# Kernel optimization log

Hardware: AMD Instinct MI355X
Metric: run time of the kernel (lower is better)

Reference implementation:

```python
import jax, jax.numpy as jnp
import numpy as np

B, H, S, D = 8, 16, 1024, 128

def setup_inputs() -> dict:
    key = jax.random.key(0)
    kq, kk, kv = jax.random.split(key, 3)
    q = jax.random.normal(kq, (B, H, S, D), dtype=jnp.float32)
    k = jax.random.normal(kk, (B, H, S, D), dtype=jnp.float32)
    v = jax.random.normal(kv, (B, H, S, D), dtype=jnp.float32)
    return {"q": q, "k": k, "v": v}

def reference(q, k, v):
    dims = q.shape[-1]
    # scores[..., j, i] = sum_k q[..., j, k] * k_[..., i, k]; note scale is 1/dims (not 1/sqrt(dims))
    scores = jnp.einsum('bhjd,bhid->bhji', q, k) / dims
    probs = jax.nn.softmax(scores, axis=-1)
    out = jnp.einsum('bhji,bhid->bhjd', probs, v)
    return out
```

## Files before the change

kernel.cpp:

```cpp
#include <hip/hip_runtime.h>

#define S_LEN 1024
#define D_DIM 128
#define KVBLK 32
#define BH_N 128

typedef __attribute__((ext_vector_type(8))) short short8;
typedef __attribute__((ext_vector_type(4))) short short4v;
typedef __attribute__((ext_vector_type(4))) float f32x4;
typedef __attribute__((ext_vector_type(16))) float f32x16;
typedef __attribute__((ext_vector_type(4))) unsigned int uint4v;

__device__ __forceinline__ unsigned short f2bf(float f) {
  union { float f; unsigned u; } x; x.f = f;
  unsigned r = x.u + 0x7fffu + ((x.u >> 16) & 1u);
  return (unsigned short)(r >> 16);
}

__device__ __forceinline__ short8 pack8(float4 a, float4 b) {
  short8 f;
  f[0] = (short)f2bf(a.x); f[1] = (short)f2bf(a.y);
  f[2] = (short)f2bf(a.z); f[3] = (short)f2bf(a.w);
  f[4] = (short)f2bf(b.x); f[5] = (short)f2bf(b.y);
  f[6] = (short)f2bf(b.z); f[7] = (short)f2bf(b.w);
  return f;
}

__device__ __forceinline__ void gload_lds16(const void* g, void* l) {
  __builtin_amdgcn_global_load_lds(
      (const __attribute__((address_space(1))) unsigned int*)g,
      (__attribute__((address_space(3))) unsigned int*)l, 16, 0, 0);
}

__device__ __forceinline__ short8 packP(const f32x16 sacc, const int c, float& l_r) {
  float p0 = exp2f(fminf(sacc[8 * c + 0], 80.f));
  float p1 = exp2f(fminf(sacc[8 * c + 1], 80.f));
  unsigned w0;
  asm("v_cvt_pk_bf16_f32 %0, %1, %2" : "=v"(w0) : "v"(p0), "v"(p1));
  float p2 = exp2f(fminf(sacc[8 * c + 2], 80.f));
  float p3 = exp2f(fminf(sacc[8 * c + 3], 80.f));
  unsigned w1;
  asm("v_cvt_pk_bf16_f32 %0, %1, %2" : "=v"(w1) : "v"(p2), "v"(p3));
  l_r += (p0 + p1) + (p2 + p3);
  float p4 = exp2f(fminf(sacc[8 * c + 4], 80.f));
  float p5 = exp2f(fminf(sacc[8 * c + 5], 80.f));
  unsigned w2;
  asm("v_cvt_pk_bf16_f32 %0, %1, %2" : "=v"(w2) : "v"(p4), "v"(p5));
  float p6 = exp2f(fminf(sacc[8 * c + 6], 80.f));
  float p7 = exp2f(fminf(sacc[8 * c + 7], 80.f));
  unsigned w3;
  asm("v_cvt_pk_bf16_f32 %0, %1, %2" : "=v"(w3) : "v"(p6), "v"(p7));
  l_r += (p4 + p5) + (p6 + p7);
  asm volatile("v_permlane32_swap_b32 %0, %1" : "+v"(w0), "+v"(w2));
  asm volatile("v_permlane32_swap_b32 %0, %1" : "+v"(w1), "+v"(w3));
  uint4v pw;
  pw[0] = w0; pw[1] = w1; pw[2] = w2; pw[3] = w3;
  return __builtin_bit_cast(short8, pw);
}

__global__ __launch_bounds__(256) void conv_k(const float* __restrict__ in,
                                              unsigned short* __restrict__ out,
                                              int n8) {
  int i = blockIdx.x * 256 + threadIdx.x;
  int stride = gridDim.x * 256;
  for (; i < n8; i += stride) {
    float4 a = ((const float4*)in)[i * 2];
    float4 b = ((const float4*)in)[i * 2 + 1];
    ((short8*)out)[i] = pack8(a, b);
  }
}

__global__ __launch_bounds__(256) void conv_vt(const float* __restrict__ v,
                                               unsigned short* __restrict__ vt) {
  __shared__ unsigned short tile[64][72];
  int b = blockIdx.x;
  int d0 = (b & 1) * 64;
  int s0 = ((b >> 1) & 15) * 64;
  int bh = b >> 5;
  int t = threadIdx.x;
  #pragma unroll
  for (int i = 0; i < 4; ++i) {
    int s = (t >> 4) + i * 16;
    int dl = (t & 15) * 4;
    float4 x = *(const float4*)(v + ((size_t)(bh * S_LEN) + s0 + s) * D_DIM + d0 + dl);
    tile[s][dl + 0] = f2bf(x.x); tile[s][dl + 1] = f2bf(x.y);
    tile[s][dl + 2] = f2bf(x.z); tile[s][dl + 3] = f2bf(x.w);
  }
  __syncthreads();
  #pragma unroll
  for (int i = 0; i < 2; ++i) {
    int j = i * 256 + t;
    int dl = j >> 3, sc = j & 7;
    short8 w;
    #pragma unroll
    for (int q = 0; q < 8; ++q) w[q] = (short)tile[sc * 8 + q][dl];
    *(short8*)(vt + ((size_t)(bh * D_DIM) + d0 + dl) * S_LEN + s0 + sc * 8) = w;
  }
}

__global__ __launch_bounds__(256, 2) void attn_main(
    const float* __restrict__ qg, const unsigned short* __restrict__ kbf,
    const unsigned short* __restrict__ vtbf, float* __restrict__ og) {
  __shared__ unsigned short K_lds[2][KVBLK * D_DIM];
  __shared__ unsigned short VT_lds[2][D_DIM * KVBLK];

  const int tid = threadIdx.x;
  const int lane = tid & 63;
  const int wid = tid >> 6;
  const int l31 = lane & 31;
  const int hi = lane >> 5;

  const int bid = blockIdx.x;
  const int bh = (bid & 7) | ((bid >> 5) << 3);
  const int qt = (bid >> 3) & 3;

  const size_t base = (size_t)bh * (S_LEN * D_DIM);
  const int qw = qt * 256 + wid * 64;

  short8 qfA[8], qfB[8];
  {
    const float s = 0.0078125f * 1.44269504088896f;
    const float* qpA = qg + base + (size_t)(qw + l31) * D_DIM + hi * 8;
    const float* qpB = qpA + 32 * D_DIM;
    #pragma unroll
    for (int c = 0; c < 8; ++c) {
      float4 a = *(const float4*)(qpA + c * 16);
      float4 b = *(const float4*)(qpA + c * 16 + 4);
      a.x *= s; a.y *= s; a.z *= s; a.w *= s;
      b.x *= s; b.y *= s; b.z *= s; b.w *= s;
      qfA[c] = pack8(a, b);
      float4 e = *(const float4*)(qpB + c * 16);
      float4 f = *(const float4*)(qpB + c * 16 + 4);
      e.x *= s; e.y *= s; e.z *= s; e.w *= s;
      f.x *= s; f.y *= s; f.z *= s; f.w *= s;
      qfB[c] = pack8(e, f);
    }
  }

  float lA = 0.f, lB = 0.f;
  f32x16 oA[4], oB[4];
  #pragma unroll
  for (int dt = 0; dt < 4; ++dt)
    #pragma unroll
    for (int r = 0; r < 16; ++r) { oA[dt][r] = 0.f; oB[dt][r] = 0.f; }

  const char* kbB = (const char*)(kbf + base);
  const char* vtB = (const char*)(vtbf + (size_t)bh * (D_DIM * S_LEN));

  int koffA, koffB, voff;
  {
    int r0 = wid * 8 + (lane >> 4);
    int c = lane & 15;
    koffA = (r0 * D_DIM + ((c ^ (r0 & 7)) * 8)) * 2;
    int r1 = r0 + 4;
    koffB = (r1 * D_DIM + ((c ^ (r1 & 7)) * 8)) * 2;
    int d0 = wid * 32 + (lane >> 2);
    int c2 = lane & 3;
    voff = (d0 * S_LEN + ((c2 ^ (lane >> 4)) * 8)) * 2;
  }
  const int KRB = l31 * 256 + ((hi ^ (l31 & 7)) << 4);
  const int VRB = l31 * 64 + ((hi ^ ((l31 >> 2) & 3)) << 4);

  #define STAGE(buf, tnext)                                                    \
    {                                                                          \
      const char* ks = kbB + (tnext) * (KVBLK * D_DIM * 2);                    \
      gload_lds16(ks + koffA, &K_lds[buf][(wid * 8) * D_DIM]);                 \
      gload_lds16(ks + koffB, &K_lds[buf][(wid * 8 + 4) * D_DIM]);             \
      const char* vs = vtB + (tnext) * (KVBLK * 2);                            \
      gload_lds16(vs + voff, &VT_lds[buf][(wid * 32) * KVBLK]);                \
      gload_lds16(vs + voff + 16 * S_LEN * 2,                                  \
                  &VT_lds[buf][(wid * 32 + 16) * KVBLK]);                      \
    }

  STAGE(0, 0);
  __syncthreads();

  for (int t = 0; t < S_LEN / KVBLK; ++t) {
    const int cur = t & 1;
    if (t + 1 < S_LEN / KVBLK) STAGE(cur ^ 1, t + 1);

    const char* kl = (const char*)&K_lds[cur][0];
    const char* vl = (const char*)&VT_lds[cur][0];

    f32x16 sA, sB;
    #pragma unroll
    for (int r = 0; r < 16; ++r) { sA[r] = 0.f; sB[r] = 0.f; }

    __builtin_amdgcn_s_setprio(1);
    #pragma unroll
    for (int c = 0; c < 8; ++c) {
      short8 kf = *(const short8*)(kl + (KRB ^ (c << 5)));
      sA = __builtin_amdgcn_mfma_f32_32x32x16_bf16(kf, qfA[c], sA, 0, 0, 0);
      sB = __builtin_amdgcn_mfma_f32_32x32x16_bf16(kf, qfB[c], sB, 0, 0, 0);
    }
    __builtin_amdgcn_s_setprio(0);

    short8 paA0 = packP(sA, 0, lA);
    short8 paA1 = packP(sA, 1, lA);
    short8 paB0 = packP(sB, 0, lB);
    short8 paB1 = packP(sB, 1, lB);

    __builtin_amdgcn_s_setprio(1);
    {
      const int vx0 = VRB;
      #pragma unroll
      for (int dt = 0; dt < 4; ++dt) {
        short8 vf = *(const short8*)(vl + vx0 + dt * 2048);
        oA[dt] = __builtin_amdgcn_mfma_f32_32x32x16_bf16(paA0, vf, oA[dt], 0, 0, 0);
        oB[dt] = __builtin_amdgcn_mfma_f32_32x32x16_bf16(paB0, vf, oB[dt], 0, 0, 0);
      }
      const int vx1 = VRB ^ 32;
      #pragma unroll
      for (int dt = 0; dt < 4; ++dt) {
        short8 vf = *(const short8*)(vl + vx1 + dt * 2048);
        oA[dt] = __builtin_amdgcn_mfma_f32_32x32x16_bf16(paA1, vf, oA[dt], 0, 0, 0);
        oB[dt] = __builtin_amdgcn_mfma_f32_32x32x16_bf16(paB1, vf, oB[dt], 0, 0, 0);
      }
    }
    __builtin_amdgcn_s_setprio(0);
    __syncthreads();
  }

  float lsA = lA + __shfl_xor(lA, 32);
  float liA = 1.0f / lsA;
  float lsB = lB + __shfl_xor(lB, 32);
  float liB = 1.0f / lsB;
  #pragma unroll
  for (int r = 0; r < 16; ++r) {
    int qr = (r & 3) + 8 * (r >> 2) + 4 * hi;
    float lvA = __shfl(liA, qr, 64);
    float lvB = __shfl(liB, qr, 64);
    #pragma unroll
    for (int dt = 0; dt < 4; ++dt) {
      og[base + (size_t)(qw + qr) * D_DIM + dt * 32 + l31] = oA[dt][r] * lvA;
      og[base + (size_t)(qw + 32 + qr) * D_DIM + dt * 32 + l31] = oB[dt][r] * lvB;
    }
  }
}

__global__ __launch_bounds__(256) void attn_fused(
    const float* __restrict__ qg, const float* __restrict__ kg,
    const float* __restrict__ vg, float* __restrict__ og) {
  __shared__ unsigned short K_lds[64 * D_DIM];
  __shared__ unsigned short VT_lds[D_DIM * 64];
  __shared__ unsigned short P_lds[4][16 * 64];

  const int tid = threadIdx.x;
  const int lane = tid & 63;
  const int wid = tid >> 6;
  const int l15 = lane & 15;
  const int lg = lane >> 4;

  const int bid = blockIdx.x;
  const int bh = (bid & 7) | ((bid >> 7) << 3);
  const int qt = (bid >> 3) & 15;

  const size_t base = (size_t)bh * (S_LEN * D_DIM);
  const int qw = qt * 64 + wid * 16;

  short8 qf[4];
  {
    const float* qp = qg + base + (size_t)(qw + l15) * D_DIM + lg * 8;
    #pragma unroll
    for (int c = 0; c < 4; ++c) {
      float4 a = *(const float4*)(qp + c * 32);
      float4 b = *(const float4*)(qp + c * 32 + 4);
      const float s = 0.0078125f;
      a.x *= s; a.y *= s; a.z *= s; a.w *= s;
      b.x *= s; b.y *= s; b.z *= s; b.w *= s;
      qf[c] = pack8(a, b);
    }
  }

  float m_r[4], l_r[4];
  f32x4 o_acc[8];
  #pragma unroll
  for (int r = 0; r < 4; ++r) { m_r[r] = -INFINITY; l_r[r] = 0.f; }
  #pragma unroll
  for (int dt = 0; dt < 8; ++dt) o_acc[dt] = (f32x4){0.f, 0.f, 0.f, 0.f};

  for (int kv0 = 0; kv0 < S_LEN; kv0 += 64) {
    {
      const float* kb = kg + base + (size_t)kv0 * D_DIM;
      #pragma unroll
      for (int c = tid; c < 64 * D_DIM / 8; c += 256) {
        int row = c >> 4, dc = c & 15;
        const float* p = kb + row * D_DIM + dc * 8;
        float4 a = *(const float4*)p;
        float4 b = *(const float4*)(p + 4);
        int sidx = row * 128 + ((dc * 8) ^ ((row & 7) << 3));
        *(short8*)&K_lds[sidx] = pack8(a, b);
      }
    }
    {
      const float* vb = vg + base + (size_t)kv0 * D_DIM;
      #pragma unroll
      for (int u = tid; u < (64 / 4) * (D_DIM / 4); u += 256) {
        int ib = u & 15;
        int db = u >> 4;
        const float* p = vb + (ib * 4) * D_DIM + db * 4;
        float rr[4][4];
        #pragma unroll
        for (int c = 0; c < 4; ++c) {
          float4 t = *(const float4*)(p + c * D_DIM);
          rr[c][0] = t.x; rr[c][1] = t.y; rr[c][2] = t.z; rr[c][3] = t.w;
        }
        #pragma unroll
        for (int j = 0; j < 4; ++j) {
          short4v w;
          w[0] = (short)f2bf(rr[0][j]); w[1] = (short)f2bf(rr[1][j]);
          w[2] = (short)f2bf(rr[2][j]); w[3] = (short)f2bf(rr[3][j]);
          int row = db * 4 + j;
          int sidx = row * 64 + ((ib * 4) ^ ((row & 7) << 3));
          *(short4v*)&VT_lds[sidx] = w;
        }
      }
    }
    __syncthreads();

    f32x4 sacc[4];
    #pragma unroll
    for (int tc = 0; tc < 4; ++tc) sacc[tc] = (f32x4){0.f, 0.f, 0.f, 0.f};
    #pragma unroll
    for (int tc = 0; tc < 4; ++tc) {
      int row = tc * 16 + l15;
      #pragma unroll
      for (int ck = 0; ck < 4; ++ck) {
        int sidx = row * 128 + ((ck * 32 + lg * 8) ^ ((row & 7) << 3));
        short8 kf = *(const short8*)&K_lds[sidx];
        sacc[tc] = __builtin_amdgcn_mfma_f32_16x16x32_bf16(qf[ck], kf, sacc[tc], 0, 0, 0);
      }
    }

    float alpha[4], ps[4];
    #pragma unroll
    for (int r = 0; r < 4; ++r) {
      float a = fmaxf(fmaxf(sacc[0][r], sacc[1][r]), fmaxf(sacc[2][r], sacc[3][r]));
      a = fmaxf(a, __shfl_xor(a, 1));
      a = fmaxf(a, __shfl_xor(a, 2));
      a = fmaxf(a, __shfl_xor(a, 4));
      a = fmaxf(a, __shfl_xor(a, 8));
      float mn = fmaxf(m_r[r], a);
      alpha[r] = __expf(m_r[r] - mn);
      m_r[r] = mn;
      ps[r] = 0.f;
    }
    #pragma unroll
    for (int tc = 0; tc < 4; ++tc) {
      #pragma unroll
      for (int r = 0; r < 4; ++r) {
        float p = __expf(sacc[tc][r] - m_r[r]);
        ps[r] += p;
        int prow = lg * 4 + r;
        int pcol = tc * 16 + l15;
        P_lds[wid][prow * 64 + (pcol ^ ((prow & 7) << 3))] = f2bf(p);
      }
    }
    #pragma unroll
    for (int r = 0; r < 4; ++r) {
      float s = ps[r];
      s += __shfl_xor(s, 1); s += __shfl_xor(s, 2);
      s += __shfl_xor(s, 4); s += __shfl_xor(s, 8);
      l_r[r] = l_r[r] * alpha[r] + s;
    }
    #pragma unroll
    for (int dt = 0; dt < 8; ++dt) {
      #pragma unroll
      for (int r = 0; r < 4; ++r) o_acc[dt][r] *= alpha[r];
    }

    #pragma unroll
    for (int kc = 0; kc < 2; ++kc) {
      int pidx = l15 * 64 + ((kc * 32 + lg * 8) ^ ((l15 & 7) << 3));
      short8 pf = *(const short8*)&P_lds[wid][pidx];
      #pragma unroll
      for (int dt = 0; dt < 8; ++dt) {
        int vrow = dt * 16 + l15;
        int vidx = vrow * 64 + ((kc * 32 + lg * 8) ^ ((vrow & 7) << 3));
        short8 vf = *(const short8*)&VT_lds[vidx];
        o_acc[dt] = __builtin_amdgcn_mfma_f32_16x16x32_bf16(pf, vf, o_acc[dt], 0, 0, 0);
      }
    }
    __syncthreads();
  }

  #pragma unroll
  for (int r = 0; r < 4; ++r) {
    float inv = 1.0f / l_r[r];
    float* op = og + base + (size_t)(qw + lg * 4 + r) * D_DIM + l15;
    #pragma unroll
    for (int dt = 0; dt < 8; ++dt) op[dt * 16] = o_acc[dt][r] * inv;
  }
}

extern "C" void kernel_launch(void* const* d_in, const int* in_sizes, int n_in,
                              void* d_out, int out_size, void* d_ws, size_t ws_size,
                              hipStream_t stream) {
  const float* q = (const float*)d_in[0];
  const float* k = (const float*)d_in[1];
  const float* v = (const float*)d_in[2];
  float* o = (float*)d_out;

  const size_t n_elem = (size_t)BH_N * S_LEN * D_DIM;
  const size_t need = 2 * n_elem * sizeof(unsigned short);

  if (ws_size >= need) {
    unsigned short* kbf = (unsigned short*)d_ws;
    unsigned short* vtbf = kbf + n_elem;
    conv_k<<<dim3(2048), dim3(256), 0, stream>>>(k, kbf, (int)(n_elem / 8));
    conv_vt<<<dim3(4096), dim3(256), 0, stream>>>(v, vtbf);
    attn_main<<<dim3(512), dim3(256), 0, stream>>>(q, kbf, vtbf, o);
  } else {
    attn_fused<<<dim3(2048), dim3(256), 0, stream>>>(q, k, v, o);
  }
}
```

Measured before the change: 152.9 us.

## Triple-buffer K/V tiles and software-pipeline QK^T ahead of PV

Moves K/V staging from a double to a triple LDS buffer and prefetches two tiles ahead. The loop is restructured so the QK^T MFMAs for the next tile are issued right after packing P for the current tile, before the current PV MFMAs. This lets softmax packing overlap with matrix work and hides global-to-LDS latency better. In exchange it uses more LDS (48KB per block), which may hurt the occupancy of two blocks per CU, adds register pressure from the live sA/sB, and drops the setprio hints.

```diff
diff --git a/kernel.cpp b/kernel.cpp
--- a/kernel.cpp
+++ b/kernel.cpp
@@ -3,6 +3,7 @@
 #define S_LEN 1024
 #define D_DIM 128
 #define KVBLK 32
+#define NT (S_LEN / KVBLK)
 #define BH_N 128
 
 typedef __attribute__((ext_vector_type(8))) short short8;
@@ -101,8 +102,8 @@
 __global__ __launch_bounds__(256, 2) void attn_main(
     const float* __restrict__ qg, const unsigned short* __restrict__ kbf,
     const unsigned short* __restrict__ vtbf, float* __restrict__ og) {
-  __shared__ unsigned short K_lds[2][KVBLK * D_DIM];
-  __shared__ unsigned short VT_lds[2][D_DIM * KVBLK];
+  __shared__ unsigned short K_lds[3][KVBLK * D_DIM];
+  __shared__ unsigned short VT_lds[3][D_DIM * KVBLK];
 
   const int tid = threadIdx.x;
   const int lane = tid & 63;
@@ -161,64 +162,87 @@
   const int KRB = l31 * 256 + ((hi ^ (l31 & 7)) << 4);
   const int VRB = l31 * 64 + ((hi ^ ((l31 >> 2) & 3)) << 4);
 
-  #define STAGE(buf, tnext)                                                    \
+  #define STAGE(slot, tnext)                                                   \
     {                                                                          \
       const char* ks = kbB + (tnext) * (KVBLK * D_DIM * 2);                    \
-      gload_lds16(ks + koffA, &K_lds[buf][(wid * 8) * D_DIM]);                 \
-      gload_lds16(ks + koffB, &K_lds[buf][(wid * 8 + 4) * D_DIM]);             \
+      gload_lds16(ks + koffA, &K_lds[slot][(wid * 8) * D_DIM]);                \
+      gload_lds16(ks + koffB, &K_lds[slot][(wid * 8 + 4) * D_DIM]);            \
       const char* vs = vtB + (tnext) * (KVBLK * 2);                            \
-      gload_lds16(vs + voff, &VT_lds[buf][(wid * 32) * KVBLK]);                \
+      gload_lds16(vs + voff, &VT_lds[slot][(wid * 32) * KVBLK]);               \
       gload_lds16(vs + voff + 16 * S_LEN * 2,                                  \
-                  &VT_lds[buf][(wid * 32 + 16) * KVBLK]);                      \
+                  &VT_lds[slot][(wid * 32 + 16) * KVBLK]);                     \
+    }
+
+  #define QKT(slot)                                                            \
+    {                                                                          \
+      const char* kl = (const char*)&K_lds[slot][0];                           \
+      f32x16 a_, b_;                                                           \
+      _Pragma("unroll")                                                        \
+      for (int r = 0; r < 16; ++r) { a_[r] = 0.f; b_[r] = 0.f; }               \
+      _Pragma("unroll")                                                        \
+      for (int c = 0; c < 8; ++c) {                                            \
+        short8 kf = *(const short8*)(kl + (KRB ^ (c << 5)));                   \
+        a_ = __builtin_amdgcn_mfma_f32_32x32x16_bf16(kf, qfA[c], a_, 0, 0, 0); \
+        b_ = __builtin_amdgcn_mfma_f32_32x32x16_bf16(kf, qfB[c], b_, 0, 0, 0); \
+      }                                                                        \
+      sA = a_; sB = b_;                                                        \
+    }
+
+  #define PV(slot)                                                             \
+    {                                                                          \
+      const char* vl = (const char*)&VT_lds[slot][0];                          \
+      _Pragma("unroll")                                                        \
+      for (int dt = 0; dt < 4; ++dt) {                                         \
+        short8 vf = *(const short8*)(vl + VRB + dt * 2048);                    \
+        oA[dt] = __builtin_amdgcn_mfma_f32_32x32x16_bf16(paA0, vf, oA[dt], 0, 0, 0); \
+        oB[dt] = __builtin_amdgcn_mfma_f32_32x32x16_bf16(paB0, vf, oB[dt], 0, 0, 0); \
+      }                                                                        \
+      _Pragma("unroll")                                                        \
+      for (int dt = 0; dt < 4; ++dt) {                                         \
+        short8 vf = *(const short8*)(vl + (VRB ^ 32) + dt * 2048);             \
+        oA[dt] = __builtin_amdgcn_mfma_f32_32x32x16_bf16(paA1, vf, oA[dt], 0, 0, 0); \
+        oB[dt] = __builtin_amdgcn_mfma_f32_32x32x16_bf16(paB1, vf, oB[dt], 0, 0, 0); \
+      }                                                                        \
     }
 
   STAGE(0, 0);
+  STAGE(1, 1);
   __syncthreads();
 
-  for (int t = 0; t < S_LEN / KVBLK; ++t) {
-    const int cur = t & 1;
-    if (t + 1 < S_LEN / KVBLK) STAGE(cur ^ 1, t + 1);
-
-    const char* kl = (const char*)&K_lds[cur][0];
-    const char* vl = (const char*)&VT_lds[cur][0];
-
-    f32x16 sA, sB;
-    #pragma unroll
-    for (int r = 0; r < 16; ++r) { sA[r] = 0.f; sB[r] = 0.f; }
-
-    __builtin_amdgcn_s_setprio(1);
-    #pragma unroll
-    for (int c = 0; c < 8; ++c) {
-      short8 kf = *(const short8*)(kl + (KRB ^ (c << 5)));
-      sA = __builtin_amdgcn_mfma_f32_32x32x16_bf16(kf, qfA[c], sA, 0, 0, 0);
-      sB = __builtin_amdgcn_mfma_f32_32x32x16_bf16(kf, qfB[c], sB, 0, 0, 0);
-    }
-    __builtin_amdgcn_s_setprio(0);
-
+  f32x16 sA, sB;
+  QKT(0);
+
+  int sl = 0;
+  for (int t = 0; t < NT - 2; ++t) {
+    int slN = sl + 1; if (slN == 3) slN = 0;
+    int slNN = slN + 1; if (slNN == 3) slNN = 0;
+    STAGE(slNN, t + 2);
     short8 paA0 = packP(sA, 0, lA);
     short8 paA1 = packP(sA, 1, lA);
     short8 paB0 = packP(sB, 0, lB);
     short8 paB1 = packP(sB, 1, lB);
-
-    __builtin_amdgcn_s_setprio(1);
-    {
-      const int vx0 = VRB;
-      #pragma unroll
-      for (int dt = 0; dt < 4; ++dt) {
-        short8 vf = *(const short8*)(vl + vx0 + dt * 2048);
-        oA[dt] = __builtin_amdgcn_mfma_f32_32x32x16_bf16(paA0, vf, oA[dt], 0, 0, 0);
-        oB[dt] = __builtin_amdgcn_mfma_f32_32x32x16_bf16(paB0, vf, oB[dt], 0, 0, 0);
-      }
-      const int vx1 = VRB ^ 32;
-      #pragma unroll
-      for (int dt = 0; dt < 4; ++dt) {
-        short8 vf = *(const short8*)(vl + vx1 + dt * 2048);
-        oA[dt] = __builtin_amdgcn_mfma_f32_32x32x16_bf16(paA1, vf, oA[dt], 0, 0, 0);
-        oB[dt] = __builtin_amdgcn_mfma_f32_32x32x16_bf16(paB1, vf, oB[dt], 0, 0, 0);
-      }
-    }
-    __builtin_amdgcn_s_setprio(0);
+    QKT(slN);
+    PV(sl);
     __syncthreads();
+    sl = slN;
+  }
+  {
+    int slN = sl + 1; if (slN == 3) slN = 0;
+    short8 paA0 = packP(sA, 0, lA);
+    short8 paA1 = packP(sA, 1, lA);
+    short8 paB0 = packP(sB, 0, lB);
+    short8 paB1 = packP(sB, 1, lB);
+    QKT(slN);
+    PV(sl);
+    __syncthreads();
+    sl = slN;
+  }
+  {
+    short8 paA0 = packP(sA, 0, lA);
+    short8 paA1 = packP(sA, 1, lA);
+    short8 paB0 = packP(sB, 0, lB);
+    short8 paB1 = packP(sB, 1, lB);
+    PV(sl);
   }
 
   float lsA = lA + __shfl_xor(lA, 32);
```

Measured after the change: 147.7 us. 1.04x faster.
